# Kernel tuning notes

Hardware: AMD Instinct MI355X
Metric: run time of the kernel (lower is better)

Reference implementation:

```python
import jax, jax.numpy as jnp
import numpy as np

EPS_IN = 1e-5   # torch InstanceNorm2d default eps
EPS_VAR = 1e-6  # clamp floor on attention-weighted variance


def _inorm(x):
    # x: (b, c, t); InstanceNorm2d with affine=False normalizes over spatial dims
    m = x.mean(axis=-1, keepdims=True)
    v = x.var(axis=-1, keepdims=True)  # biased variance, matches torch eval-mode IN
    return (x - m) / jnp.sqrt(v + EPS_IN)


def setup_inputs() -> dict:
    key = jax.random.key(0)
    ks = jax.random.split(key, 9)
    b, t, d = 4, 4096, 256
    sc = 1.0 / np.sqrt(d).astype(np.float32)
    return {
        "fc": jax.random.normal(ks[0], (b, t, d), jnp.float32),
        "fs": jax.random.normal(ks[1], (b, t, d), jnp.float32),
        "fcs": jax.random.normal(ks[2], (b, t, d), jnp.float32),
        "Wf": jax.random.normal(ks[3], (d, d), jnp.float32) * sc,
        "bf": jax.random.normal(ks[4], (d,), jnp.float32) * 0.01,
        "Wg": jax.random.normal(ks[5], (d, d), jnp.float32) * sc,
        "bg": jax.random.normal(ks[6], (d,), jnp.float32) * 0.01,
        "Wh": jax.random.normal(ks[7], (d, d), jnp.float32) * sc,
        "bh": jax.random.normal(ks[8], (d,), jnp.float32) * 0.01,
    }


def reference(fc, fs, fcs, Wf, bf, Wg, bg, Wh, bh):
    # (b, t, d) -> channel-first flat (b, d, t); 1x1 conv == per-token linear
    fc_t = jnp.swapaxes(fc, 1, 2)
    fs_t = jnp.swapaxes(fs, 1, 2)
    fcs_t = jnp.swapaxes(fcs, 1, 2)

    Q = jnp.einsum('oc,bct->bto', Wf, _inorm(fc_t)) + bf                 # (b,t,d)
    K = jnp.einsum('oc,bct->bot', Wg, _inorm(fs_t)) + bg[None, :, None]  # (b,d,t)
    V = jnp.einsum('oc,bct->bto', Wh, fs_t) + bh                         # (b,t,d)

    A = jax.nn.softmax(jnp.einsum('btd,bdu->btu', Q, K), axis=-1)        # (b,t,t)
    M = jnp.einsum('btu,bud->btd', A, V)                                 # mean
    Var = jnp.einsum('btu,bud->btd', A, V * V) - M * M                   # E[v^2]-E[v]^2
    S = jnp.sqrt(jnp.maximum(Var, EPS_VAR))

    out_t = jnp.swapaxes(S, 1, 2) * _inorm(fcs_t) + jnp.swapaxes(M, 1, 2)  # (b,d,t)
    return jnp.swapaxes(out_t, 1, 2)  # (b, t, d)
```

## Files before the change

kernel.cpp:

```cpp
#include <hip/hip_runtime.h>
#include <math.h>

#define B 4
#define T 4096
#define D 256
#define NCH 16
#define CHT (T / NCH)
#define KC 32
#define NCHUNK (T / KC)

typedef __attribute__((ext_vector_type(8))) _Float16 half8;
typedef __attribute__((ext_vector_type(4))) _Float16 half4;
typedef __attribute__((ext_vector_type(4))) float f32x4;

__global__ __launch_bounds__(256) void k_prep(
    const float* __restrict__ fc, const float* __restrict__ fs,
    const float* __restrict__ fcs, float* __restrict__ part,
    const float* __restrict__ Wf, const float* __restrict__ Wg,
    const float* __restrict__ Wh, _Float16* __restrict__ Whi,
    _Float16* __restrict__ Wlo)
{
    int blk = blockIdx.x;
    if (blk < 192) {
        int tensor = blk / (B * NCH);
        int rem = blk % (B * NCH);
        int b = rem / NCH, ch = rem % NCH;
        const float* x = (tensor == 0) ? fc : ((tensor == 1) ? fs : fcs);
        int c = threadIdx.x;
        const float* p = x + ((size_t)b * T + (size_t)ch * CHT) * D + c;
        float s = 0.f, ss = 0.f;
        for (int t = 0; t < CHT; ++t) {
            float v = p[(size_t)t * D];
            s += v; ss += v * v;
        }
        float* o = part + (((size_t)tensor * B + b) * NCH + ch) * 2 * D;
        o[c] = s;
        o[D + c] = ss;
    } else {
        int base = (blk - 192) * 2048;
        #pragma unroll
        for (int i = 0; i < 8; ++i) {
            int idx = base + threadIdx.x + i * 256;
            int which = idx >> 16, rc = idx & 65535;
            const float* Wsrc = (which == 0) ? Wf : ((which == 1) ? Wg : Wh);
            float v = Wsrc[rc];
            _Float16 h = (_Float16)v;
            float l = v - (float)h;
            Whi[idx] = h;
            Wlo[idx] = (_Float16)l;
        }
    }
}

__global__ __launch_bounds__(256) void k_stats_final(
    const float* __restrict__ part, float* __restrict__ stats)
{
    int blk = blockIdx.x;
    int tensor = blk / B, b = blk % B;
    int c = threadIdx.x;
    const float* pp = part + (((size_t)tensor * B + b) * NCH) * 2 * D;
    float s = 0.f, ss = 0.f;
    for (int ch = 0; ch < NCH; ++ch) {
        s  += pp[(size_t)ch * 2 * D + c];
        ss += pp[(size_t)ch * 2 * D + D + c];
    }
    float mean = s / (float)T;
    float var  = ss / (float)T - mean * mean;
    float rstd = rsqrtf(var + 1e-5f);
    float* st = stats + (size_t)tensor * 2 * B * D;
    st[(size_t)b * D + c]          = mean;
    st[(size_t)B * D + b * D + c]  = rstd;
}

__global__ __launch_bounds__(256) void k_gemm3(
    const float* __restrict__ fc, const float* __restrict__ fs,
    const _Float16* __restrict__ Whi, const _Float16* __restrict__ Wlo,
    const float* __restrict__ bf, const float* __restrict__ bg,
    const float* __restrict__ bh, const float* __restrict__ stats,
    _Float16* __restrict__ Qg, _Float16* __restrict__ Kg,
    _Float16* __restrict__ oV, _Float16* __restrict__ oV2h,
    _Float16* __restrict__ oV2l)
{
    __shared__ _Float16 Xl[64 * 256];
    const int which = blockIdx.x >> 8;
    const int m0 = (blockIdx.x & 255) * 64;
    const int b = m0 / T;
    const int tid = threadIdx.x;
    const float* x = (which == 0) ? fc : fs;
    const float* bias = (which == 0) ? bf : ((which == 1) ? bg : bh);
    const _Float16* Wh_ = Whi + which * 65536;
    const _Float16* Wl_ = Wlo + which * 65536;
    const int use_norm = (which != 2);
    const float* mean = stats + (which == 0 ? 0 : 1) * 2 * B * D;
    const float* rstd = mean + B * D;

    #pragma unroll
    for (int j = 0; j < 16; ++j) {
        int idx = tid + j * 256;
        int m = idx >> 6, c4 = idx & 63;
        float4 v = *(const float4*)(x + ((size_t)(m0 + m)) * D + c4 * 4);
        if (use_norm) {
            int c = c4 * 4;
            v.x = (v.x - mean[b * D + c + 0]) * rstd[b * D + c + 0];
            v.y = (v.y - mean[b * D + c + 1]) * rstd[b * D + c + 1];
            v.z = (v.z - mean[b * D + c + 2]) * rstd[b * D + c + 2];
            v.w = (v.w - mean[b * D + c + 3]) * rstd[b * D + c + 3];
        }
        half4 h;
        h[0] = (_Float16)v.x; h[1] = (_Float16)v.y;
        h[2] = (_Float16)v.z; h[3] = (_Float16)v.w;
        *(half4*)&Xl[m * 256 + ((c4 * 4) ^ ((m & 7) << 3))] = h;
    }
    __syncthreads();

    const int l = tid & 63, w = tid >> 6;
    const int lo16 = l & 15, hi4 = l >> 4;
    const int row = w * 16 + lo16;

    float bias_v[16];
    #pragma unroll
    for (int nt = 0; nt < 16; ++nt) bias_v[nt] = bias[nt * 16 + lo16];

    f32x4 acc[16];
    #pragma unroll
    for (int nt = 0; nt < 16; ++nt) acc[nt] = (f32x4){0.f, 0.f, 0.f, 0.f};

    #pragma unroll
    for (int kk = 0; kk < 8; ++kk) {
        half8 a = *(const half8*)&Xl[row * 256 + ((kk * 32 + hi4 * 8) ^ ((row & 7) << 3))];
        #pragma unroll
        for (int nt = 0; nt < 16; ++nt) {
            size_t wo = (size_t)(nt * 16 + lo16) * 256 + kk * 32 + hi4 * 8;
            half8 bhf = *(const half8*)(Wh_ + wo);
            acc[nt] = __builtin_amdgcn_mfma_f32_16x16x32_f16(a, bhf, acc[nt], 0, 0, 0);
            half8 blf = *(const half8*)(Wl_ + wo);
            acc[nt] = __builtin_amdgcn_mfma_f32_16x16x32_f16(a, blf, acc[nt], 0, 0, 0);
        }
    }

    if (which != 2) {
        _Float16* out1 = (which == 0) ? Qg : Kg;
        #pragma unroll
        for (int nt = 0; nt < 16; ++nt)
            #pragma unroll
            for (int r = 0; r < 4; ++r) {
                int t = m0 + w * 16 + hi4 * 4 + r;
                out1[(size_t)t * D + nt * 16 + lo16] = (_Float16)(acc[nt][r] + bias_v[nt]);
            }
    } else {
        int t0 = (m0 % T) + w * 16 + hi4 * 4;
        #pragma unroll
        for (int nt = 0; nt < 16; ++nt) {
            int o = nt * 16 + lo16;
            half4 vh, h4, l4;
            #pragma unroll
            for (int r = 0; r < 4; ++r) {
                float v = acc[nt][r] + bias_v[nt];
                _Float16 vhh = (_Float16)v;
                float f2 = (float)vhh * (float)vhh;
                _Float16 hh = (_Float16)f2;
                float fl = f2 - (float)hh;
                vh[r] = vhh; h4[r] = hh; l4[r] = (_Float16)fl;
            }
            size_t base = ((size_t)b * D + o) * T + t0;
            *(half4*)(oV   + base) = vh;
            *(half4*)(oV2h + base) = h4;
            *(half4*)(oV2l + base) = l4;
        }
    }
}

__global__ __launch_bounds__(512, 1) void k_attn(
    const _Float16* __restrict__ Qg, const _Float16* __restrict__ Kg,
    const _Float16* __restrict__ Vtg, const _Float16* __restrict__ V2hg,
    const _Float16* __restrict__ V2lg, const float* __restrict__ fcs,
    const float* __restrict__ stats_fcs, float* __restrict__ out)
{
    __shared__ __align__(16) _Float16 Kl [2][32 * 256];
    __shared__ __align__(16) _Float16 Vl [2][256 * 32];
    __shared__ __align__(16) _Float16 V2h[2][256 * 32];
    __shared__ __align__(16) _Float16 V2l[2][256 * 32];
    __shared__ __align__(16) _Float16 Pl[64 * 32];
    __shared__ float corr_lds[64];
    __shared__ float l_lds[64];
    __shared__ int   flags[4];

    const int tid = threadIdx.x;
    const int l = tid & 63;
    const int w = tid >> 6;
    const int swz = (blockIdx.x & 7) * 32 + (blockIdx.x >> 3);
    const int b  = swz >> 6;
    const int q0 = (swz & 63) << 6;
    const int lo16 = l & 15, hi4 = l >> 4;

    const _Float16* KgB  = Kg   + (size_t)b * T * D;
    const _Float16* VtB  = Vtg  + (size_t)b * D * T;
    const _Float16* V2hB = V2hg + (size_t)b * D * T;
    const _Float16* V2lB = V2lg + (size_t)b * D * T;

    half8 qf[8];
    if (w < 4) {
        const _Float16* qp = Qg + ((size_t)(b * T + q0 + 16 * w + lo16)) * D + hi4 * 8;
        #pragma unroll
        for (int kk = 0; kk < 8; ++kk) qf[kk] = *(const half8*)(qp + kk * 32);
    }

    f32x4 accM[4][2], accE[4][2];
    #pragma unroll
    for (int qs = 0; qs < 4; ++qs)
        #pragma unroll
        for (int jj = 0; jj < 2; ++jj) {
            accM[qs][jj] = (f32x4){0.f, 0.f, 0.f, 0.f};
            accE[qs][jj] = (f32x4){0.f, 0.f, 0.f, 0.f};
        }
    float m_run[4] = {-1e9f, -1e9f, -1e9f, -1e9f};
    float lv[4] = {0.f, 0.f, 0.f, 0.f};

    auto stage = [&](int kcs, int cb) {
        int k0 = kcs * KC;
        int t2 = tid & 255;
        half8 kr[4], vr[4], vhr[4], vlr[4];
        #pragma unroll
        for (int i = 0; i < 4; ++i) {
            int g = t2 + i * 256;
            kr[i] = *(const half8*)(KgB + (size_t)(k0 + (g >> 5)) * D + (g & 31) * 8);
        }
        #pragma unroll
        for (int i = 0; i < 4; ++i) {
            int g = t2 + i * 256; int d = g >> 2, kg = g & 3;
            size_t off = (size_t)d * T + k0 + kg * 8;
            vr[i]  = *(const half8*)(VtB  + off);
            vhr[i] = *(const half8*)(V2hB + off);
            vlr[i] = *(const half8*)(V2lB + off);
        }
        #pragma unroll
        for (int i = 0; i < 4; ++i) {
            int g = t2 + i * 256; int rr = g >> 5, cg = g & 31;
            *(half8*)&Kl[cb][rr * 256 + ((cg ^ (rr & 7)) << 3)] = kr[i];
        }
        #pragma unroll
        for (int i = 0; i < 4; ++i) {
            int g = t2 + i * 256; int d = g >> 2, kg = g & 3;
            int p = d * 32 + ((kg ^ ((d >> 1) & 3)) << 3);
            *(half8*)&Vl[cb][p]  = vr[i];
            *(half8*)&V2h[cb][p] = vhr[i];
            *(half8*)&V2l[cb][p] = vlr[i];
        }
    };

    if (w >= 4) stage(0, 0);
    __syncthreads();
    int cur = 0;

    for (int kc = 0; kc < NCHUNK; ++kc) {
        if (w < 4) {
            f32x4 c0 = (f32x4){0.f, 0.f, 0.f, 0.f}, c1 = (f32x4){0.f, 0.f, 0.f, 0.f};
            __builtin_amdgcn_s_setprio(1);
            #pragma unroll
            for (int kk = 0; kk < 8; ++kk) {
                int cg = kk * 4 + hi4;
                half8 b0 = *(const half8*)&Kl[cur][lo16 * 256 + ((cg ^ (lo16 & 7)) << 3)];
                half8 b1 = *(const half8*)&Kl[cur][(16 + lo16) * 256 + ((cg ^ ((16 + lo16) & 7)) << 3)];
                c0 = __builtin_amdgcn_mfma_f32_16x16x32_f16(qf[kk], b0, c0, 0, 0, 0);
                c1 = __builtin_amdgcn_mfma_f32_16x16x32_f16(qf[kk], b1, c1, 0, 0, 0);
            }
            __builtin_amdgcn_s_setprio(0);

            float cm[4];
            #pragma unroll
            for (int r = 0; r < 4; ++r) cm[r] = fmaxf(c0[r], c1[r]);
            float tmax = fmaxf(fmaxf(cm[0] - m_run[0], cm[1] - m_run[1]),
                               fmaxf(cm[2] - m_run[2], cm[3] - m_run[3]));
            int flagv = 0;
            if (__any(tmax > 10.f)) {
                flagv = 1;
                float corr[4];
                #pragma unroll
                for (int r = 0; r < 4; ++r) {
                    float rm = cm[r];
                    rm = fmaxf(rm, __shfl_xor(rm, 1));
                    rm = fmaxf(rm, __shfl_xor(rm, 2));
                    rm = fmaxf(rm, __shfl_xor(rm, 4));
                    rm = fmaxf(rm, __shfl_xor(rm, 8));
                    float mn = fmaxf(m_run[r], rm);
                    corr[r] = __expf(m_run[r] - mn);
                    m_run[r] = mn;
                    lv[r] *= corr[r];
                }
                if (lo16 == 0) {
                    #pragma unroll
                    for (int r = 0; r < 4; ++r)
                        corr_lds[w * 16 + hi4 * 4 + r] = corr[r];
                }
            }
            if (l == 0) flags[w] = flagv;

            float p0[4], p1[4];
            #pragma unroll
            for (int r = 0; r < 4; ++r) {
                p0[r] = __expf(c0[r] - m_run[r]);
                p1[r] = __expf(c1[r] - m_run[r]);
                lv[r] += p0[r] + p1[r];
            }
            #pragma unroll
            for (int r = 0; r < 4; ++r) {
                int q = 16 * w + hi4 * 4 + r;
                int ka = lo16, kb = 16 + lo16;
                Pl[q * 32 + (((ka >> 3) ^ (q & 3)) << 3) + (ka & 7)] = (_Float16)p0[r];
                Pl[q * 32 + (((kb >> 3) ^ (q & 3)) << 3) + (kb & 7)] = (_Float16)p1[r];
            }
        } else {
            if (kc + 1 < NCHUNK) stage(kc + 1, cur ^ 1);
        }
        __syncthreads();

        #pragma unroll
        for (int qs = 0; qs < 4; ++qs) {
            if (flags[qs]) {
                #pragma unroll
                for (int r = 0; r < 4; ++r) {
                    float c = corr_lds[qs * 16 + hi4 * 4 + r];
                    accM[qs][0][r] *= c; accM[qs][1][r] *= c;
                    accE[qs][0][r] *= c; accE[qs][1][r] *= c;
                }
            }
        }

        half8 pa[4];
        #pragma unroll
        for (int qs = 0; qs < 4; ++qs) {
            int q = qs * 16 + lo16;
            pa[qs] = *(const half8*)&Pl[q * 32 + ((hi4 ^ (q & 3)) << 3)];
        }

        __builtin_amdgcn_s_setprio(1);
        #pragma unroll
        for (int jj = 0; jj < 2; ++jj) {
            int d = (2 * w + jj) * 16 + lo16;
            int p = d * 32 + ((hi4 ^ ((d >> 1) & 3)) << 3);
            half8 bh  = *(const half8*)&Vl[cur][p];
            half8 b2h = *(const half8*)&V2h[cur][p];
            half8 b2l = *(const half8*)&V2l[cur][p];
            #pragma unroll
            for (int qs = 0; qs < 4; ++qs) {
                accM[qs][jj] = __builtin_amdgcn_mfma_f32_16x16x32_f16(pa[qs], bh,  accM[qs][jj], 0, 0, 0);
                accE[qs][jj] = __builtin_amdgcn_mfma_f32_16x16x32_f16(pa[qs], b2h, accE[qs][jj], 0, 0, 0);
                accE[qs][jj] = __builtin_amdgcn_mfma_f32_16x16x32_f16(pa[qs], b2l, accE[qs][jj], 0, 0, 0);
            }
        }
        __builtin_amdgcn_s_setprio(0);

        __syncthreads();
        cur ^= 1;
    }

    if (w < 4) {
        #pragma unroll
        for (int r = 0; r < 4; ++r) {
            float lr = lv[r];
            lr += __shfl_xor(lr, 1);
            lr += __shfl_xor(lr, 2);
            lr += __shfl_xor(lr, 4);
            lr += __shfl_xor(lr, 8);
            if (lo16 == 0) l_lds[w * 16 + hi4 * 4 + r] = lr;
        }
    }
    __syncthreads();

    const float* mfc = stats_fcs;
    const float* rfc = stats_fcs + B * D;
    #pragma unroll
    for (int qs = 0; qs < 4; ++qs) {
        #pragma unroll
        for (int r = 0; r < 4; ++r) {
            float linv = 1.f / l_lds[qs * 16 + hi4 * 4 + r];
            int q = q0 + qs * 16 + hi4 * 4 + r;
            size_t rowb = ((size_t)(b * T + q)) * D;
            #pragma unroll
            for (int jj = 0; jj < 2; ++jj) {
                int d = (2 * w + jj) * 16 + lo16;
                float M  = accM[qs][jj][r] * linv;
                float E2 = accE[qs][jj][r] * linv;
                float S  = sqrtf(fmaxf(E2 - M * M, 1e-6f));
                float f  = fcs[rowb + d];
                out[rowb + d] = S * ((f - mfc[b * D + d]) * rfc[b * D + d]) + M;
            }
        }
    }
}

extern "C" void kernel_launch(void* const* d_in, const int* in_sizes, int n_in,
                              void* d_out, int out_size, void* d_ws, size_t ws_size,
                              hipStream_t stream)
{
    const float* fc  = (const float*)d_in[0];
    const float* fs  = (const float*)d_in[1];
    const float* fcs = (const float*)d_in[2];
    const float* Wf  = (const float*)d_in[3];
    const float* bf  = (const float*)d_in[4];
    const float* Wg  = (const float*)d_in[5];
    const float* bg  = (const float*)d_in[6];
    const float* Wh  = (const float*)d_in[7];
    const float* bh  = (const float*)d_in[8];
    float* out = (float*)d_out;

    char* ws = (char*)d_ws;
    float* stats = (float*)ws;
    float* part  = (float*)(ws + (64 << 10));
    _Float16* Whi = (_Float16*)(ws + (512 << 10));
    _Float16* Wlo = Whi + 3 * 65536;
    _Float16* Qg   = (_Float16*)(ws + (2 << 20));
    _Float16* Kg   = Qg  + (size_t)B * T * D;
    _Float16* Vtg  = Kg  + (size_t)B * T * D;
    _Float16* V2hg = Vtg + (size_t)B * T * D;
    _Float16* V2lg = V2hg + (size_t)B * T * D;

    k_prep<<<288, 256, 0, stream>>>(fc, fs, fcs, part, Wf, Wg, Wh, Whi, Wlo);
    k_stats_final<<<3 * B, 256, 0, stream>>>(part, stats);

    float* st_fcs = stats + 2 * 2 * B * D;

    k_gemm3<<<3 * 256, 256, 0, stream>>>(fc, fs, Whi, Wlo, bf, bg, bh, stats,
                                         Qg, Kg, Vtg, V2hg, V2lg);

    k_attn<<<B * (T / 64), 512, 0, stream>>>(Qg, Kg, Vtg, V2hg, V2lg, fcs, st_fcs, out);
}
```

Before: 356.2 us.

## Double attention block to 16 waves, split PV columns and staging across more waves

The attention kernel now runs 1024 threads per block instead of 512. Each of the 16 waves owns a single 16-column d-slice for the PV and variance MFMAs. The 12 non-QK waves now share the K/V/V2 staging loads as a flattened 4096-item work list. This halves each wave's accumulator registers and spreads the load and MFMA work over more waves to hide latency better. In exchange, the launch bound of 1024 threads with 4 blocks per SM cannot be met on a CU, so it may force very tight register limits and spilling; the staging also gains branchy per-item address selection.

```diff
diff --git a/kernel.cpp b/kernel.cpp
--- a/kernel.cpp
+++ b/kernel.cpp
@@ -170,7 +170,7 @@
     }
 }
 
-__global__ __launch_bounds__(512, 1) void k_attn(
+__global__ __launch_bounds__(1024, 4) void k_attn(
     const _Float16* __restrict__ Qg, const _Float16* __restrict__ Kg,
     const _Float16* __restrict__ Vtg, const _Float16* __restrict__ V2hg,
     const _Float16* __restrict__ V2lg, const float* __restrict__ fcs,
@@ -205,46 +205,47 @@
         for (int kk = 0; kk < 8; ++kk) qf[kk] = *(const half8*)(qp + kk * 32);
     }
 
-    f32x4 accM[4][2], accE[4][2];
-    #pragma unroll
-    for (int qs = 0; qs < 4; ++qs)
-        #pragma unroll
-        for (int jj = 0; jj < 2; ++jj) {
-            accM[qs][jj] = (f32x4){0.f, 0.f, 0.f, 0.f};
-            accE[qs][jj] = (f32x4){0.f, 0.f, 0.f, 0.f};
-        }
+    f32x4 accM[4], accE[4];
+    #pragma unroll
+    for (int qs = 0; qs < 4; ++qs) {
+        accM[qs] = (f32x4){0.f, 0.f, 0.f, 0.f};
+        accE[qs] = (f32x4){0.f, 0.f, 0.f, 0.f};
+    }
     float m_run[4] = {-1e9f, -1e9f, -1e9f, -1e9f};
     float lv[4] = {0.f, 0.f, 0.f, 0.f};
 
+    const int st = tid - 256;
     auto stage = [&](int kcs, int cb) {
         int k0 = kcs * KC;
-        int t2 = tid & 255;
-        half8 kr[4], vr[4], vhr[4], vlr[4];
-        #pragma unroll
-        for (int i = 0; i < 4; ++i) {
-            int g = t2 + i * 256;
-            kr[i] = *(const half8*)(KgB + (size_t)(k0 + (g >> 5)) * D + (g & 31) * 8);
-        }
-        #pragma unroll
-        for (int i = 0; i < 4; ++i) {
-            int g = t2 + i * 256; int d = g >> 2, kg = g & 3;
-            size_t off = (size_t)d * T + k0 + kg * 8;
-            vr[i]  = *(const half8*)(VtB  + off);
-            vhr[i] = *(const half8*)(V2hB + off);
-            vlr[i] = *(const half8*)(V2lB + off);
-        }
-        #pragma unroll
-        for (int i = 0; i < 4; ++i) {
-            int g = t2 + i * 256; int rr = g >> 5, cg = g & 31;
-            *(half8*)&Kl[cb][rr * 256 + ((cg ^ (rr & 7)) << 3)] = kr[i];
-        }
-        #pragma unroll
-        for (int i = 0; i < 4; ++i) {
-            int g = t2 + i * 256; int d = g >> 2, kg = g & 3;
-            int p = d * 32 + ((kg ^ ((d >> 1) & 3)) << 3);
-            *(half8*)&Vl[cb][p]  = vr[i];
-            *(half8*)&V2h[cb][p] = vhr[i];
-            *(half8*)&V2l[cb][p] = vlr[i];
+        half8 r[6];
+        #pragma unroll
+        for (int i = 0; i < 6; ++i) {
+            int g = st + i * 768;
+            if (g < 4096) {
+                int s = g >> 10, u = g & 1023;
+                const _Float16* src;
+                size_t off;
+                if (s == 0) { int row = u >> 5, cg = u & 31; off = (size_t)(k0 + row) * D + cg * 8; src = KgB; }
+                else { int d = u >> 2, kg = u & 3; off = (size_t)d * T + k0 + kg * 8;
+                       src = (s == 1) ? VtB : ((s == 2) ? V2hB : V2lB); }
+                r[i] = *(const half8*)(src + off);
+            }
+        }
+        #pragma unroll
+        for (int i = 0; i < 6; ++i) {
+            int g = st + i * 768;
+            if (g < 4096) {
+                int s = g >> 10, u = g & 1023;
+                if (s == 0) {
+                    int row = u >> 5, cg = u & 31;
+                    *(half8*)&Kl[cb][row * 256 + ((cg ^ (row & 7)) << 3)] = r[i];
+                } else {
+                    int d = u >> 2, kg = u & 3;
+                    int p = d * 32 + ((kg ^ ((d >> 1) & 3)) << 3);
+                    _Float16* dst = (s == 1) ? &Vl[cb][0] : ((s == 2) ? &V2h[cb][0] : &V2l[cb][0]);
+                    *(half8*)&dst[p] = r[i];
+                }
+            }
         }
     };
 
@@ -320,8 +321,7 @@
                 #pragma unroll
                 for (int r = 0; r < 4; ++r) {
                     float c = corr_lds[qs * 16 + hi4 * 4 + r];
-                    accM[qs][0][r] *= c; accM[qs][1][r] *= c;
-                    accE[qs][0][r] *= c; accE[qs][1][r] *= c;
+                    accM[qs][r] *= c; accE[qs][r] *= c;
                 }
             }
         }
@@ -333,22 +333,21 @@
             pa[qs] = *(const half8*)&Pl[q * 32 + ((hi4 ^ (q & 3)) << 3)];
         }
 
-        __builtin_amdgcn_s_setprio(1);
-        #pragma unroll
-        for (int jj = 0; jj < 2; ++jj) {
-            int d = (2 * w + jj) * 16 + lo16;
+        {
+            int d = w * 16 + lo16;
             int p = d * 32 + ((hi4 ^ ((d >> 1) & 3)) << 3);
             half8 bh  = *(const half8*)&Vl[cur][p];
             half8 b2h = *(const half8*)&V2h[cur][p];
             half8 b2l = *(const half8*)&V2l[cur][p];
+            __builtin_amdgcn_s_setprio(1);
             #pragma unroll
             for (int qs = 0; qs < 4; ++qs) {
-                accM[qs][jj] = __builtin_amdgcn_mfma_f32_16x16x32_f16(pa[qs], bh,  accM[qs][jj], 0, 0, 0);
-                accE[qs][jj] = __builtin_amdgcn_mfma_f32_16x16x32_f16(pa[qs], b2h, accE[qs][jj], 0, 0, 0);
-                accE[qs][jj] = __builtin_amdgcn_mfma_f32_16x16x32_f16(pa[qs], b2l, accE[qs][jj], 0, 0, 0);
-            }
-        }
-        __builtin_amdgcn_s_setprio(0);
+                accM[qs] = __builtin_amdgcn_mfma_f32_16x16x32_f16(pa[qs], bh,  accM[qs], 0, 0, 0);
+                accE[qs] = __builtin_amdgcn_mfma_f32_16x16x32_f16(pa[qs], b2h, accE[qs], 0, 0, 0);
+                accE[qs] = __builtin_amdgcn_mfma_f32_16x16x32_f16(pa[qs], b2l, accE[qs], 0, 0, 0);
+            }
+            __builtin_amdgcn_s_setprio(0);
+        }
 
         __syncthreads();
         cur ^= 1;
@@ -376,15 +375,12 @@
             float linv = 1.f / l_lds[qs * 16 + hi4 * 4 + r];
             int q = q0 + qs * 16 + hi4 * 4 + r;
             size_t rowb = ((size_t)(b * T + q)) * D;
-            #pragma unroll
-            for (int jj = 0; jj < 2; ++jj) {
-                int d = (2 * w + jj) * 16 + lo16;
-                float M  = accM[qs][jj][r] * linv;
-                float E2 = accE[qs][jj][r] * linv;
-                float S  = sqrtf(fmaxf(E2 - M * M, 1e-6f));
-                float f  = fcs[rowb + d];
-                out[rowb + d] = S * ((f - mfc[b * D + d]) * rfc[b * D + d]) + M;
-            }
+            int d = w * 16 + lo16;
+            float M  = accM[qs][r] * linv;
+            float E2 = accE[qs][r] * linv;
+            float S  = sqrtf(fmaxf(E2 - M * M, 1e-6f));
+            float f  = fcs[rowb + d];
+            out[rowb + d] = S * ((f - mfc[b * D + d]) * rfc[b * D + d]) + M;
         }
     }
 }
@@ -423,5 +419,5 @@
     k_gemm3<<<3 * 256, 256, 0, stream>>>(fc, fs, Whi, Wlo, bf, bg, bh, stats,
                                          Qg, Kg, Vtg, V2hg, V2lg);
 
-    k_attn<<<B * (T / 64), 512, 0, stream>>>(Qg, Kg, Vtg, V2hg, V2lg, fcs, st_fcs, out);
+    k_attn<<<B * (T / 64), 1024, 0, stream>>>(Qg, Kg, Vtg, V2hg, V2lg, fcs, st_fcs, out);
 }
```

Result: slower. 453.4 us (+27.3%).

## Software-pipeline PV of previous chunk with QK of current chunk, single barrier

Applied to the files above, without the earlier changes.

Restructures the attention loop so each iteration runs QK^T and softmax for chunk kc while the PV/PV² MFMAs consume chunk kc-1 from double-buffered P, correction and flag arrays. This removes the second __syncthreads per iteration. K is still prefetched one chunk ahead, while V tiles are now staged into the same-index buffer just in time. The aim is to overlap softmax latency with matrix work and halve the barrier count. In exchange it uses more LDS and more live registers per thread, and it adds an epilogue PV call.

```diff
diff --git a/kernel.cpp b/kernel.cpp
--- a/kernel.cpp
+++ b/kernel.cpp
@@ -180,10 +180,10 @@
     __shared__ __align__(16) _Float16 Vl [2][256 * 32];
     __shared__ __align__(16) _Float16 V2h[2][256 * 32];
     __shared__ __align__(16) _Float16 V2l[2][256 * 32];
-    __shared__ __align__(16) _Float16 Pl[64 * 32];
-    __shared__ float corr_lds[64];
+    __shared__ __align__(16) _Float16 Pl [2][64 * 32];
+    __shared__ float corr_lds[2][64];
     __shared__ float l_lds[64];
-    __shared__ int   flags[4];
+    __shared__ int   flags[2][4];
 
     const int tid = threadIdx.x;
     const int l = tid & 63;
@@ -216,55 +216,76 @@
     float m_run[4] = {-1e9f, -1e9f, -1e9f, -1e9f};
     float lv[4] = {0.f, 0.f, 0.f, 0.f};
 
-    auto stage = [&](int kcs, int cb) {
-        int k0 = kcs * KC;
-        int t2 = tid & 255;
-        half8 kr[4], vr[4], vhr[4], vlr[4];
+    const int t2 = tid & 255;
+
+    auto do_pv = [&](int pb) {
+        #pragma unroll
+        for (int qs = 0; qs < 4; ++qs) {
+            if (flags[pb][qs]) {
+                #pragma unroll
+                for (int r = 0; r < 4; ++r) {
+                    float c = corr_lds[pb][qs * 16 + hi4 * 4 + r];
+                    accM[qs][0][r] *= c; accM[qs][1][r] *= c;
+                    accE[qs][0][r] *= c; accE[qs][1][r] *= c;
+                }
+            }
+        }
+        half8 pa[4];
+        #pragma unroll
+        for (int qs = 0; qs < 4; ++qs) {
+            int q = qs * 16 + lo16;
+            pa[qs] = *(const half8*)&Pl[pb][q * 32 + ((hi4 ^ (q & 3)) << 3)];
+        }
+        __builtin_amdgcn_s_setprio(1);
+        #pragma unroll
+        for (int jj = 0; jj < 2; ++jj) {
+            int d = (2 * w + jj) * 16 + lo16;
+            int p = d * 32 + ((hi4 ^ ((d >> 1) & 3)) << 3);
+            half8 bh  = *(const half8*)&Vl[pb][p];
+            half8 b2h = *(const half8*)&V2h[pb][p];
+            half8 b2l = *(const half8*)&V2l[pb][p];
+            #pragma unroll
+            for (int qs = 0; qs < 4; ++qs) {
+                accM[qs][jj] = __builtin_amdgcn_mfma_f32_16x16x32_f16(pa[qs], bh,  accM[qs][jj], 0, 0, 0);
+                accE[qs][jj] = __builtin_amdgcn_mfma_f32_16x16x32_f16(pa[qs], b2h, accE[qs][jj], 0, 0, 0);
+                accE[qs][jj] = __builtin_amdgcn_mfma_f32_16x16x32_f16(pa[qs], b2l, accE[qs][jj], 0, 0, 0);
+            }
+        }
+        __builtin_amdgcn_s_setprio(0);
+    };
+
+    if (w >= 4) {
+        half8 kr0[4];
         #pragma unroll
         for (int i = 0; i < 4; ++i) {
             int g = t2 + i * 256;
-            kr[i] = *(const half8*)(KgB + (size_t)(k0 + (g >> 5)) * D + (g & 31) * 8);
-        }
-        #pragma unroll
-        for (int i = 0; i < 4; ++i) {
-            int g = t2 + i * 256; int d = g >> 2, kg = g & 3;
-            size_t off = (size_t)d * T + k0 + kg * 8;
-            vr[i]  = *(const half8*)(VtB  + off);
-            vhr[i] = *(const half8*)(V2hB + off);
-            vlr[i] = *(const half8*)(V2lB + off);
+            kr0[i] = *(const half8*)(KgB + (size_t)(g >> 5) * D + (g & 31) * 8);
         }
         #pragma unroll
         for (int i = 0; i < 4; ++i) {
             int g = t2 + i * 256; int rr = g >> 5, cg = g & 31;
-            *(half8*)&Kl[cb][rr * 256 + ((cg ^ (rr & 7)) << 3)] = kr[i];
-        }
-        #pragma unroll
-        for (int i = 0; i < 4; ++i) {
-            int g = t2 + i * 256; int d = g >> 2, kg = g & 3;
-            int p = d * 32 + ((kg ^ ((d >> 1) & 3)) << 3);
-            *(half8*)&Vl[cb][p]  = vr[i];
-            *(half8*)&V2h[cb][p] = vhr[i];
-            *(half8*)&V2l[cb][p] = vlr[i];
-        }
-    };
-
-    if (w >= 4) stage(0, 0);
+            *(half8*)&Kl[0][rr * 256 + ((cg ^ (rr & 7)) << 3)] = kr0[i];
+        }
+    }
     __syncthreads();
-    int cur = 0;
 
     for (int kc = 0; kc < NCHUNK; ++kc) {
+        const int cb = kc & 1, pb = cb ^ 1;
+
         if (w < 4) {
             f32x4 c0 = (f32x4){0.f, 0.f, 0.f, 0.f}, c1 = (f32x4){0.f, 0.f, 0.f, 0.f};
             __builtin_amdgcn_s_setprio(1);
             #pragma unroll
             for (int kk = 0; kk < 8; ++kk) {
                 int cg = kk * 4 + hi4;
-                half8 b0 = *(const half8*)&Kl[cur][lo16 * 256 + ((cg ^ (lo16 & 7)) << 3)];
-                half8 b1 = *(const half8*)&Kl[cur][(16 + lo16) * 256 + ((cg ^ ((16 + lo16) & 7)) << 3)];
+                half8 b0 = *(const half8*)&Kl[cb][lo16 * 256 + ((cg ^ (lo16 & 7)) << 3)];
+                half8 b1 = *(const half8*)&Kl[cb][(16 + lo16) * 256 + ((cg ^ ((16 + lo16) & 7)) << 3)];
                 c0 = __builtin_amdgcn_mfma_f32_16x16x32_f16(qf[kk], b0, c0, 0, 0, 0);
                 c1 = __builtin_amdgcn_mfma_f32_16x16x32_f16(qf[kk], b1, c1, 0, 0, 0);
             }
             __builtin_amdgcn_s_setprio(0);
+
+            if (kc > 0) do_pv(pb);
 
             float cm[4];
             #pragma unroll
@@ -290,10 +311,10 @@
                 if (lo16 == 0) {
                     #pragma unroll
                     for (int r = 0; r < 4; ++r)
-                        corr_lds[w * 16 + hi4 * 4 + r] = corr[r];
-                }
-            }
-            if (l == 0) flags[w] = flagv;
+                        corr_lds[cb][w * 16 + hi4 * 4 + r] = corr[r];
+                }
+            }
+            if (l == 0) flags[cb][w] = flagv;
 
             float p0[4], p1[4];
             #pragma unroll
@@ -306,53 +327,54 @@
             for (int r = 0; r < 4; ++r) {
                 int q = 16 * w + hi4 * 4 + r;
                 int ka = lo16, kb = 16 + lo16;
-                Pl[q * 32 + (((ka >> 3) ^ (q & 3)) << 3) + (ka & 7)] = (_Float16)p0[r];
-                Pl[q * 32 + (((kb >> 3) ^ (q & 3)) << 3) + (kb & 7)] = (_Float16)p1[r];
+                Pl[cb][q * 32 + (((ka >> 3) ^ (q & 3)) << 3) + (ka & 7)] = (_Float16)p0[r];
+                Pl[cb][q * 32 + (((kb >> 3) ^ (q & 3)) << 3) + (kb & 7)] = (_Float16)p1[r];
             }
         } else {
-            if (kc + 1 < NCHUNK) stage(kc + 1, cur ^ 1);
+            half8 kr[4], vr[4], vhr[4], vlr[4];
+            const bool doK = (kc + 1 < NCHUNK);
+            if (doK) {
+                int kn = (kc + 1) * KC;
+                #pragma unroll
+                for (int i = 0; i < 4; ++i) {
+                    int g = t2 + i * 256;
+                    kr[i] = *(const half8*)(KgB + (size_t)(kn + (g >> 5)) * D + (g & 31) * 8);
+                }
+            }
+            {
+                int k0 = kc * KC;
+                #pragma unroll
+                for (int i = 0; i < 4; ++i) {
+                    int g = t2 + i * 256; int d = g >> 2, kg = g & 3;
+                    size_t off = (size_t)d * T + k0 + kg * 8;
+                    vr[i]  = *(const half8*)(VtB  + off);
+                    vhr[i] = *(const half8*)(V2hB + off);
+                    vlr[i] = *(const half8*)(V2lB + off);
+                }
+            }
+
+            if (kc > 0) do_pv(pb);
+
+            if (doK) {
+                #pragma unroll
+                for (int i = 0; i < 4; ++i) {
+                    int g = t2 + i * 256; int rr = g >> 5, cg = g & 31;
+                    *(half8*)&Kl[cb ^ 1][rr * 256 + ((cg ^ (rr & 7)) << 3)] = kr[i];
+                }
+            }
+            #pragma unroll
+            for (int i = 0; i < 4; ++i) {
+                int g = t2 + i * 256; int d = g >> 2, kg = g & 3;
+                int p = d * 32 + ((kg ^ ((d >> 1) & 3)) << 3);
+                *(half8*)&Vl[cb][p]  = vr[i];
+                *(half8*)&V2h[cb][p] = vhr[i];
+                *(half8*)&V2l[cb][p] = vlr[i];
+            }
         }
         __syncthreads();
-
-        #pragma unroll
-        for (int qs = 0; qs < 4; ++qs) {
-            if (flags[qs]) {
-                #pragma unroll
-                for (int r = 0; r < 4; ++r) {
-                    float c = corr_lds[qs * 16 + hi4 * 4 + r];
-                    accM[qs][0][r] *= c; accM[qs][1][r] *= c;
-                    accE[qs][0][r] *= c; accE[qs][1][r] *= c;
-                }
-            }
-        }
-
-        half8 pa[4];
-        #pragma unroll
-        for (int qs = 0; qs < 4; ++qs) {
-            int q = qs * 16 + lo16;
-            pa[qs] = *(const half8*)&Pl[q * 32 + ((hi4 ^ (q & 3)) << 3)];
-        }
-
-        __builtin_amdgcn_s_setprio(1);
-        #pragma unroll
-        for (int jj = 0; jj < 2; ++jj) {
-            int d = (2 * w + jj) * 16 + lo16;
-            int p = d * 32 + ((hi4 ^ ((d >> 1) & 3)) << 3);
-            half8 bh  = *(const half8*)&Vl[cur][p];
-            half8 b2h = *(const half8*)&V2h[cur][p];
-            half8 b2l = *(const half8*)&V2l[cur][p];
-            #pragma unroll
-            for (int qs = 0; qs < 4; ++qs) {
-                accM[qs][jj] = __builtin_amdgcn_mfma_f32_16x16x32_f16(pa[qs], bh,  accM[qs][jj], 0, 0, 0);
-                accE[qs][jj] = __builtin_amdgcn_mfma_f32_16x16x32_f16(pa[qs], b2h, accE[qs][jj], 0, 0, 0);
-                accE[qs][jj] = __builtin_amdgcn_mfma_f32_16x16x32_f16(pa[qs], b2l, accE[qs][jj], 0, 0, 0);
-            }
-        }
-        __builtin_amdgcn_s_setprio(0);
-
-        __syncthreads();
-        cur ^= 1;
-    }
+    }
+
+    do_pv((NCHUNK - 1) & 1);
 
     if (w < 4) {
         #pragma unroll
```

Result: faster. 320.9 us (-9.9%).
